# Performance work log

Hardware: AMD Instinct MI355X
Metric: run time of the kernel (lower is better)

The kernel has to match this reference:

```python
import jax, jax.numpy as jnp
import numpy as np
from jax.scipy.special import ndtr

# ---- constants matching init_kwargs ----
DF = 4.0            # fixed_df (closed-form Student-t4 quantile used)
EWMA_ALPHA = 0.94
SCALE_EPS = 1e-5
T_STEPS = 50        # diff_steps
BETA_START = 1e-4
BETA_END = 0.1
L = 6               # residual_layers
C = 32              # residual_channels
EMB = 512           # diffusion step-embedding width


def _t4_ppf(u):
    """Exact Student-t(df=4) quantile (Shaw closed form); u in (0,1)."""
    a = jnp.clip(4.0 * u * (1.0 - u), 1e-12, 1.0)
    r = jnp.sqrt(a)
    q = 2.0 * jnp.sqrt(jnp.maximum(jnp.cos(jnp.arccos(r) / 3.0) / r - 1.0, 0.0))
    return jnp.sign(u - 0.5) * q


def _forward(x_hist, z_init, noise, w_in, b_in, temb_w1, temb_b1, temb_w2, temb_b2,
             lyr_wt, lyr_bt, lyr_wdil, lyr_bdil, lyr_wout, lyr_bout,
             w_o1, b_o1, w_o2, b_o2, num_samples):
    B, Tc, D = x_hist.shape
    S = num_samples
    # ---- Student-t marginal fit (EWMA variance recurrence as lax.scan) ----
    loc = jnp.mean(x_hist, axis=1, keepdims=True)              # [B,1,D]
    c2 = (x_hist - loc) ** 2                                    # [B,Tc,D]
    def ewma_step(v, c):
        return EWMA_ALPHA * v + (1.0 - EWMA_ALPHA) * c, None
    v_last, _ = jax.lax.scan(ewma_step, c2[:, 0, :], jnp.swapaxes(c2[:, 1:, :], 0, 1))
    scale_f = jnp.maximum(jnp.sqrt(v_last * (DF - 2.0) / DF), SCALE_EPS)  # [B,D]

    # ---- DDPM schedule (linear betas) ----
    betas = jnp.linspace(BETA_START, BETA_END, T_STEPS).astype(jnp.float32)
    alphas = 1.0 - betas
    abar = jnp.cumprod(alphas)
    abar_prev = jnp.concatenate([jnp.ones((1,), jnp.float32), abar[:-1]])
    coef_x0 = betas * jnp.sqrt(abar_prev) / (1.0 - abar)
    coef_xt = (1.0 - abar_prev) * jnp.sqrt(alphas) / (1.0 - abar)
    post_var = betas * (1.0 - abar_prev) / (1.0 - abar)
    sqrt_ab = jnp.sqrt(abar)
    sqrt_1mab = jnp.sqrt(1.0 - abar)

    half = jnp.arange(64, dtype=jnp.float32)

    def eps_net(x, t):
        # diffusion-step embedding
        e = t.astype(jnp.float32) * 10.0 ** (half * 4.0 / 63.0)
        pe = jnp.concatenate([jnp.sin(e), jnp.cos(e)])          # [128]
        te = jax.nn.silu(pe @ temb_w1 + temb_b1)
        te = jax.nn.silu(te @ temb_w2 + temb_b2)                # [EMB]
        h = jax.nn.relu(jnp.einsum('cd,bdh->bch', w_in, x) + b_in[:, None])
        skip = jnp.zeros_like(h)
        for i in range(L):
            cond = te @ lyr_wt[i] + lyr_bt[i]                   # [C]
            d = 2 ** i
            y = jax.lax.conv_general_dilated(
                h + cond[None, :, None], lyr_wdil[i], (1,), [(d, d)],
                rhs_dilation=(d,), dimension_numbers=('NCH', 'OIH', 'NCH')
            ) + lyr_bdil[i][None, :, None]                       # [B,2C,H]
            gate, filt = jnp.split(y, 2, axis=1)
            y = jnp.tanh(filt) * jax.nn.sigmoid(gate)            # [B,C,H]
            y = jnp.einsum('oc,bch->boh', lyr_wout[i], y) + lyr_bout[i][None, :, None]
            res, sk = jnp.split(y, 2, axis=1)
            h = (h + res) * (1.0 / np.sqrt(2.0))
            skip = skip + sk
        s = jax.nn.relu(jnp.einsum('oc,bch->boh', w_o1, skip * (1.0 / np.sqrt(L))) + b_o1[:, None])
        return jnp.einsum('dc,bch->bdh', w_o2, s) + b_o2[:, None]

    @jax.checkpoint
    def ddpm_step(x, inp):
        t, nz = inp
        eps = eps_net(x, t)
        x0 = jnp.clip((x - sqrt_1mab[t] * eps) / sqrt_ab[t], -1.0, 1.0)  # clip_denoised
        mean = coef_x0[t] * x0 + coef_xt[t] * x
        x = mean + jnp.where(t > 0, jnp.sqrt(post_var[t]), 0.0) * nz
        return x, None

    ts = jnp.arange(T_STEPS - 1, -1, -1)
    z, _ = jax.lax.scan(ddpm_step, z_init, (ts, noise))          # [S*B,D,H]
    H = z.shape[-1]
    z = z.reshape(S, B, D, H).transpose(0, 1, 3, 2)              # [S,B,H,D]

    # ---- Gaussian -> Student-t marginal transform ----
    u = jnp.clip(ndtr(z), 1e-6, 1.0 - 1e-6)
    t_std = _t4_ppf(u)
    return loc[None] + scale_f[None, :, None, :] * t_std          # [S,B,H,D]


def setup_inputs() -> dict:
    key = jax.random.key(0)
    ks = jax.random.split(key, 12)
    D, Tc, H, B, S = 128, 192, 24, 32, 16
    p = lambda k, sh: jax.random.normal(k, sh, jnp.float32) * 0.05
    z = lambda sh: jnp.zeros(sh, jnp.float32)
    return {
        'x_hist': jax.random.normal(ks[0], (B, Tc, D), jnp.float32),
        'z_init': jax.random.normal(ks[1], (S * B, D, H), jnp.float32),
        'noise': jax.random.normal(ks[2], (T_STEPS, S * B, D, H), jnp.float32),
        'w_in': p(ks[3], (C, D)), 'b_in': z((C,)),
        'temb_w1': p(ks[4], (128, EMB)), 'temb_b1': z((EMB,)),
        'temb_w2': p(ks[5], (EMB, EMB)), 'temb_b2': z((EMB,)),
        'lyr_wt': p(ks[6], (L, EMB, C)), 'lyr_bt': z((L, C)),
        'lyr_wdil': p(ks[7], (L, 2 * C, C, 3)), 'lyr_bdil': z((L, 2 * C)),
        'lyr_wout': p(ks[8], (L, 2 * C, C)), 'lyr_bout': z((L, 2 * C)),
        'w_o1': p(ks[9], (C, C)), 'b_o1': z((C,)),
        'w_o2': p(ks[10], (D, C)), 'b_o2': z((D,)),
        'num_samples': 16,
    }


def reference(x_hist, z_init, noise, w_in, b_in, temb_w1, temb_b1, temb_w2, temb_b2,
              lyr_wt, lyr_bt, lyr_wdil, lyr_bdil, lyr_wout, lyr_bout,
              w_o1, b_o1, w_o2, b_o2, num_samples):
    return _forward(x_hist, z_init, noise, w_in, b_in, temb_w1, temb_b1, temb_w2, temb_b2,
                    lyr_wt, lyr_bt, lyr_wdil, lyr_bdil, lyr_wout, lyr_bout,
                    w_o1, b_o1, w_o2, b_o2, num_samples)
```

## Files before the change

kernel.cpp:

```cpp
#include <hip/hip_runtime.h>
#include <math.h>

#define T_STEPS 50
#define NB 512
#define RS2 0.70710678118654752f
#define INV_SQRT_L 0.40824829046386302f
#define WPACK_SHORT_OFF 36864

struct SchedArg { float cx0[T_STEPS], cxt[T_STEPS], sig[T_STEPS], s1m[T_STEPS], isab[T_STEPS]; };
struct FreqArg  { double f[64]; };

typedef short bf16x8 __attribute__((ext_vector_type(8)));
typedef float f32x4  __attribute__((ext_vector_type(4)));

__device__ __forceinline__ float4 ld4s(const float* p) { return *reinterpret_cast<const float4*>(p); }
__device__ __forceinline__ void   st4s(float* p, float4 v) { *reinterpret_cast<float4*>(p) = v; }
__device__ __forceinline__ float4 ld4g(const float* __restrict__ p) { return *reinterpret_cast<const float4*>(p); }
__device__ __forceinline__ float fast_sig(float x)  { return 1.f / (1.f + __expf(-x)); }
__device__ __forceinline__ float fast_tanh(float x) { float e = __expf(2.f * x); return 1.f - 2.f / (e + 1.f); }

__device__ __forceinline__ unsigned rne1(float f) {
    unsigned u = __float_as_uint(f);
    return (u + 0x7FFFu + ((u >> 16) & 1u)) >> 16;
}
__device__ __forceinline__ unsigned pk2(float a, float b) {
    unsigned r;
    asm("v_cvt_pk_bf16_f32 %0, %1, %2" : "=v"(r) : "v"(a), "v"(b));
    return r;
}
__device__ __forceinline__ void st_bf4(short* p, float a, float b, float c, float d) {
    uint2 v; v.x = pk2(a, b); v.y = pk2(c, d);
    *reinterpret_cast<uint2*>(p) = v;
}
__device__ __forceinline__ f32x4 mma(bf16x8 a, bf16x8 b, f32x4 c) {
    return __builtin_amdgcn_mfma_f32_16x16x32_bf16(a, b, c, 0, 0, 0);
}
__device__ __forceinline__ f32x4 bias4s(const float* p) {
    float4 b = ld4s(p);
    f32x4 r; r[0] = b.x; r[1] = b.y; r[2] = b.z; r[3] = b.w;
    return r;
}
__device__ __forceinline__ bf16x8 ldfrag(const short* p) {
    return *reinterpret_cast<const bf16x8*>(p);
}

__global__ __launch_bounds__(256) void fit_kernel(const float* __restrict__ xh,
                                                  float* __restrict__ loc,
                                                  float* __restrict__ scalef) {
    int gid = blockIdx.x * 256 + threadIdx.x;
    int b = gid >> 7, d = gid & 127;
    const float* p = xh + (size_t)b * 192 * 128 + d;
    float s = 0.f;
    for (int t = 0; t < 192; ++t) s += p[t * 128];
    float m = s * (1.0f / 192.0f);
    float v = 0.f;
    for (int t = 0; t < 192; ++t) {
        float c = p[t * 128] - m; c *= c;
        v = (t == 0) ? c : 0.94f * v + (1.0f - 0.94f) * c;
    }
    loc[gid] = m;
    scalef[gid] = fmaxf(sqrtf(v * 0.5f), 1e-5f);
}

__global__ __launch_bounds__(256) void temb_kernel(
    const float* __restrict__ w1, const float* __restrict__ b1,
    const float* __restrict__ w2, const float* __restrict__ b2,
    const float* __restrict__ wt, const float* __restrict__ bt,
    float* __restrict__ cond_all, FreqArg fq) {
    int t = blockIdx.x;
    int tid = threadIdx.x;
    __shared__ float pe[128], te1[512], te2[512];
    if (tid < 64) {
        double e = (double)t * fq.f[tid];
        pe[tid]      = (float)sin(e);
        pe[tid + 64] = (float)cos(e);
    }
    __syncthreads();
    for (int j = tid; j < 512; j += 256) {
        float acc = b1[j];
        for (int k = 0; k < 128; ++k) acc += pe[k] * w1[k * 512 + j];
        te1[j] = acc / (1.f + expf(-acc));
    }
    __syncthreads();
    for (int j = tid; j < 512; j += 256) {
        float acc = b2[j];
        for (int k = 0; k < 512; ++k) acc += te1[k] * w2[k * 512 + j];
        te2[j] = acc / (1.f + expf(-acc));
    }
    __syncthreads();
    if (tid < 192) {
        int l = tid >> 5, c = tid & 31;
        float acc = bt[l * 32 + c];
        const float* w = wt + (size_t)l * 512 * 32 + c;
        for (int k = 0; k < 512; ++k) acc += te2[k] * w[k * 32];
        cond_all[t * 192 + tid] = acc;
    }
}

__global__ __launch_bounds__(256) void prep_kernel(
    const float* __restrict__ w_in, const float* __restrict__ lyr_wdil,
    const float* __restrict__ lyr_wout, const float* __restrict__ w_o1,
    const float* __restrict__ w_o2, short* __restrict__ wpack) {
    int gid = blockIdx.x * 256 + threadIdx.x;
    if (gid >= 58368) return;
    int j = gid & 7, l = (gid >> 3) & 63, frag = gid >> 9;
    int m = l & 15, k = (l >> 4) * 8 + j;
    float v;
    if (frag < 8) {
        int m2 = frag >> 2, ks = frag & 3;
        v = w_in[(m2 * 16 + m) * 128 + ks * 32 + k];
    } else if (frag < 80) {
        int fi = frag - 8;
        int li = fi / 12, rem = fi % 12;
        int mg = rem / 6, rem2 = rem % 6;
        int tp = rem2 >> 1, gf = rem2 & 1;
        int o = gf * 32 + mg * 16 + m;
        v = lyr_wdil[((li * 64 + o) * 32 + k) * 3 + tp];
    } else if (frag < 104) {
        int fi = frag - 80;
        int li = fi >> 2, mo = fi & 3;
        v = lyr_wout[li * 2048 + (mo * 16 + m) * 32 + k];
    } else if (frag < 106) {
        int m2 = frag - 104;
        v = w_o1[(m2 * 16 + m) * 32 + k] * INV_SQRT_L;
    } else {
        int m8 = frag - 106;
        v = w_o2[(m8 * 16 + m) * 32 + k];
    }
    wpack[gid] = (short)rne1(v);
}

__global__ __launch_bounds__(256, 2) void diffusion_kernel(
    const float* __restrict__ z_init, const float* __restrict__ noise,
    const float* __restrict__ b_in,  const float* __restrict__ lyr_bdil,
    const float* __restrict__ lyr_bout, const float* __restrict__ b_o1,
    const float* __restrict__ b_o2, const float* __restrict__ cond_all,
    const short* __restrict__ wpack, const float* __restrict__ loc,
    const float* __restrict__ scalef, float* __restrict__ out, SchedArg sc) {

    __shared__ __align__(16) short xbB[32 * 136];
    __shared__ __align__(16) short hcB[33 * 40];
    __shared__ __align__(16) short actB[32 * 40];
    __shared__ __align__(16) short skB[32 * 40];
    __shared__ __align__(16) float biasB[960];
    __shared__ __align__(16) float condB[2][192];

    const int tid = threadIdx.x;
    const int wv  = __builtin_amdgcn_readfirstlane(tid >> 6);
    const int l   = tid & 63;
    const int ln  = l & 15;
    const int lq  = l >> 4;
    const int bb  = blockIdx.x;

    const short* wpP1 = wpack;
    const short* wpCv = wpack + 4096;
    const short* wpWo = wpack + 40960;
    const short* wpO1 = wpack + 53248;
    const short* wpO2 = wpack + 54272;

    const int mh   = wv >> 1;
    const int nn   = wv & 1;
    const int colw = nn * 16 + ln;
    const bool cvw = (colw < 24);

    bf16x8 aP1[4], aCv[6][3][2], aO1, aWoR[5], aWoS[6], aO2[2];
#pragma unroll
    for (int ks = 0; ks < 4; ++ks)
        aP1[ks] = ldfrag(wpP1 + (mh * 4 + ks) * 512 + l * 8);
    aO1 = ldfrag(wpO1 + mh * 512 + l * 8);
#pragma unroll
    for (int li = 0; li < 6; ++li) {
#pragma unroll
        for (int tp = 0; tp < 3; ++tp) {
            if (li == 5 && tp != 1) continue;
#pragma unroll
            for (int gf = 0; gf < 2; ++gf)
                aCv[li][tp][gf] = ldfrag(wpCv + (li * 12 + mh * 6 + tp * 2 + gf) * 512 + l * 8);
        }
        if (li < 5) aWoR[li] = ldfrag(wpWo + (li * 4 + mh) * 512 + l * 8);
        aWoS[li] = ldfrag(wpWo + (li * 4 + 2 + mh) * 512 + l * 8);
    }
    aO2[0] = ldfrag(wpO2 + wv * 512 + l * 8);
    aO2[1] = ldfrag(wpO2 + (wv + 4) * 512 + l * 8);

    for (int i = tid; i < 3072; i += 256) {
        int d = i / 24, h = i - d * 24;
        xbB[h * 136 + d] = (short)rne1(z_init[(size_t)bb * 3072 + i]);
    }
    for (int i = tid; i < 1088; i += 256) xbB[24 * 136 + i] = 0;
    for (int i = tid; i < 960; i += 256) {
        float v;
        if      (i < 32)  v = b_in[i];
        else if (i < 416) v = lyr_bdil[i - 32];
        else if (i < 800) v = lyr_bout[i - 416];
        else if (i < 832) v = b_o1[i - 800];
        else              v = b_o2[i - 832];
        biasB[i] = v;
    }
    if (tid < 192) condB[0][tid] = cond_all[(T_STEPS - 1) * 192 + tid];
    if (tid < 40) hcB[32 * 40 + tid] = 0;

    f32x4 xr[2][2];
#pragma unroll
    for (int mi = 0; mi < 2; ++mi)
#pragma unroll
        for (int n = 0; n < 2; ++n) {
            const int col = n * 16 + ln;
            const int d0 = (wv + 4 * mi) * 16 + lq * 4;
#pragma unroll
            for (int i = 0; i < 4; ++i)
                xr[mi][n][i] = (col < 24) ? z_init[(size_t)bb * 3072 + (d0 + i) * 24 + col] : 0.f;
        }
    __syncthreads();

    for (int step = 0; step < T_STEPS; ++step) {
        const int t = T_STEPS - 1 - step;
        const float* cnd = condB[step & 1];

        float cndnext = 0.f;
        if (step + 1 < T_STEPS && tid < 192)
            cndnext = cond_all[(t - 1) * 192 + tid];

        f32x4 hr;
        {
            f32x4 acc = bias4s(biasB + mh * 16 + lq * 4);
            const short* xb = xbB + colw * 136;
#pragma unroll
            for (int ks = 0; ks < 4; ++ks)
                acc = mma(aP1[ks], ldfrag(xb + ks * 32 + lq * 8), acc);
#pragma unroll
            for (int i = 0; i < 4; ++i) acc[i] = fmaxf(acc[i], 0.f);
            hr = acc;
            float4 cv = ld4s(cnd + mh * 16 + lq * 4);
            st_bf4(hcB + colw * 40 + mh * 16 + lq * 4,
                   hr[0] + cv.x, hr[1] + cv.y, hr[2] + cv.z, hr[3] + cv.w);
        }
        f32x4 skr;
#pragma unroll
        for (int i = 0; i < 4; ++i) skr[i] = 0.f;
        __syncthreads();

#pragma unroll
        for (int li = 0; li < 6; ++li) {
            const int dd = 1 << li;
            {
                f32x4 accg = bias4s(biasB + 32 + li * 64 + mh * 16 + lq * 4);
                f32x4 accf = bias4s(biasB + 32 + li * 64 + 32 + mh * 16 + lq * 4);
#pragma unroll
                for (int tp = 0; tp < 3; ++tp) {
                    if (li == 5 && tp != 1) continue;
                    int hh = colw + (tp - 1) * dd;
                    int colp = ((unsigned)hh < 24u) ? hh : 32;
                    bf16x8 b = ldfrag(hcB + colp * 40 + lq * 8);
                    accg = mma(aCv[li][tp][0], b, accg);
                    accf = mma(aCv[li][tp][1], b, accf);
                }
                st_bf4(actB + colw * 40 + mh * 16 + lq * 4,
                       fast_tanh(accf[0]) * fast_sig(accg[0]),
                       fast_tanh(accf[1]) * fast_sig(accg[1]),
                       fast_tanh(accf[2]) * fast_sig(accg[2]),
                       fast_tanh(accf[3]) * fast_sig(accg[3]));
            }
            __syncthreads();

            {
                bf16x8 b = ldfrag(actB + colw * 40 + lq * 8);
                if (li < 5) {
                    f32x4 accR = mma(aWoR[li], b,
                                     bias4s(biasB + 416 + li * 64 + mh * 16 + lq * 4));
#pragma unroll
                    for (int i = 0; i < 4; ++i) hr[i] = (hr[i] + accR[i]) * RS2;
                    float4 cv = ld4s(cnd + (li + 1) * 32 + mh * 16 + lq * 4);
                    st_bf4(hcB + colw * 40 + mh * 16 + lq * 4,
                           hr[0] + cv.x, hr[1] + cv.y, hr[2] + cv.z, hr[3] + cv.w);
                }
                f32x4 accS = mma(aWoS[li], b,
                                 bias4s(biasB + 416 + li * 64 + (2 + mh) * 16 + lq * 4));
#pragma unroll
                for (int i = 0; i < 4; ++i) skr[i] += accS[i];
                if (li == 5)
                    st_bf4(skB + colw * 40 + mh * 16 + lq * 4,
                           skr[0], skr[1], skr[2], skr[3]);
            }
            __syncthreads();
        }

        {
            f32x4 acc = bias4s(biasB + 800 + mh * 16 + lq * 4);
            acc = mma(aO1, ldfrag(skB + colw * 40 + lq * 8), acc);
            st_bf4(actB + colw * 40 + mh * 16 + lq * 4,
                   fmaxf(acc[0], 0.f), fmaxf(acc[1], 0.f),
                   fmaxf(acc[2], 0.f), fmaxf(acc[3], 0.f));
        }
        __syncthreads();

        {
            const float cx0 = sc.cx0[t], cxt = sc.cxt[t], sig = sc.sig[t];
            const float s1m = sc.s1m[t], isab = sc.isab[t];
#pragma unroll
            for (int mi = 0; mi < 2; ++mi) {
                const int d0 = (wv + 4 * mi) * 16 + lq * 4;
                f32x4 bia = bias4s(biasB + 832 + d0);
#pragma unroll
                for (int n = 0; n < 2; ++n) {
                    const int col = n * 16 + ln;
                    f32x4 acc = mma(aO2[mi], ldfrag(actB + col * 40 + lq * 8), bia);
                    if (col < 24) {
                        const float* nzp = noise + ((size_t)step * NB + bb) * 3072 + col;
                        float xn[4];
#pragma unroll
                        for (int i = 0; i < 4; ++i) {
                            float xv = xr[mi][n][i];
                            float nz = nzp[(d0 + i) * 24];
                            float x0 = fminf(fmaxf((xv - s1m * acc[i]) * isab, -1.f), 1.f);
                            xn[i] = cx0 * x0 + cxt * xv + sig * nz;
                            xr[mi][n][i] = xn[i];
                        }
                        st_bf4(xbB + col * 136 + d0, xn[0], xn[1], xn[2], xn[3]);
                    }
                }
            }
            if (step + 1 < T_STEPS && tid < 192)
                condB[(step + 1) & 1][tid] = cndnext;
        }
        __syncthreads();
    }

    {
        const int b = bb & 31;
#pragma unroll
        for (int mi = 0; mi < 2; ++mi) {
#pragma unroll
            for (int n = 0; n < 2; ++n) {
                const int col = n * 16 + ln;
                if (col >= 24) continue;
                const int d0 = (wv + 4 * mi) * 16 + lq * 4;
                float4 l4 = ld4g(loc + b * 128 + d0);
                float4 s4 = ld4g(scalef + b * 128 + d0);
                float4 o4;
#pragma unroll
                for (int e = 0; e < 4; ++e) {
                    float z = xr[mi][n][e];
                    float u = 0.5f * (1.f + erff(z * RS2));
                    u = fminf(fmaxf(u, 1e-6f), 1.f - 1e-6f);
                    float a4 = fminf(fmaxf(4.f * u * (1.f - u), 1e-12f), 1.f);
                    float rr = sqrtf(a4);
                    float q2 = 2.f * sqrtf(fmaxf(cosf(acosf(rr) * (1.f / 3.f)) / rr - 1.f, 0.f));
                    float tstd = (u < 0.5f) ? -q2 : q2;
                    (&o4.x)[e] = (&l4.x)[e] + (&s4.x)[e] * tstd;
                }
                *reinterpret_cast<float4*>(out + (size_t)bb * 3072 + col * 128 + d0) = o4;
            }
        }
    }
}

extern "C" void kernel_launch(void* const* d_in, const int* in_sizes, int n_in,
                              void* d_out, int out_size, void* d_ws, size_t ws_size,
                              hipStream_t stream) {
    const float* x_hist  = (const float*)d_in[0];
    const float* z_init  = (const float*)d_in[1];
    const float* noise   = (const float*)d_in[2];
    const float* w_in    = (const float*)d_in[3];
    const float* b_in    = (const float*)d_in[4];
    const float* temb_w1 = (const float*)d_in[5];
    const float* temb_b1 = (const float*)d_in[6];
    const float* temb_w2 = (const float*)d_in[7];
    const float* temb_b2 = (const float*)d_in[8];
    const float* lyr_wt  = (const float*)d_in[9];
    const float* lyr_bt  = (const float*)d_in[10];
    const float* lyr_wdil= (const float*)d_in[11];
    const float* lyr_bdil= (const float*)d_in[12];
    const float* lyr_wout= (const float*)d_in[13];
    const float* lyr_bout= (const float*)d_in[14];
    const float* w_o1    = (const float*)d_in[15];
    const float* b_o1    = (const float*)d_in[16];
    const float* w_o2    = (const float*)d_in[17];
    const float* b_o2    = (const float*)d_in[18];
    float* out = (float*)d_out;

    float* loc      = (float*)d_ws;
    float* scalef   = loc + 4096;
    float* cond_all = scalef + 4096;
    short* wpack    = (short*)d_ws + WPACK_SHORT_OFF;

    SchedArg sa;
    double abar = 1.0;
    for (int t = 0; t < T_STEPS; ++t) {
        double beta  = 1e-4 + (0.1 - 1e-4) * ((double)t / 49.0);
        double alpha = 1.0 - beta;
        double abprev = abar;
        abar *= alpha;
        sa.cx0[t]  = (float)(beta * sqrt(abprev) / (1.0 - abar));
        sa.cxt[t]  = (float)((1.0 - abprev) * sqrt(alpha) / (1.0 - abar));
        double pv  = beta * (1.0 - abprev) / (1.0 - abar);
        sa.sig[t]  = (t > 0) ? (float)sqrt(pv) : 0.f;
        sa.s1m[t]  = (float)sqrt(1.0 - abar);
        sa.isab[t] = (float)(1.0 / sqrt(abar));
    }
    FreqArg fa;
    for (int j = 0; j < 64; ++j) fa.f[j] = pow(10.0, (double)j * 4.0 / 63.0);

    prep_kernel<<<228, 256, 0, stream>>>(w_in, lyr_wdil, lyr_wout, w_o1, w_o2, wpack);
    fit_kernel<<<16, 256, 0, stream>>>(x_hist, loc, scalef);
    temb_kernel<<<T_STEPS, 256, 0, stream>>>(temb_w1, temb_b1, temb_w2, temb_b2,
                                             lyr_wt, lyr_bt, cond_all, fa);
    diffusion_kernel<<<NB, 256, 0, stream>>>(z_init, noise, b_in, lyr_bdil,
                                             lyr_bout, b_o1, b_o2, cond_all,
                                             wpack, loc, scalef, out, sa);
}
```

Baseline: 488.2 us.

## Process two sample rows per block to halve grid and amortize barriers

Each block now handles two independent sample/batch rows, with double LDS buffers and duplicated register state, and the grid shrinks from 512 to 256 blocks. The point is to interleave two independent MFMA chains between each pair of barriers, hiding latency and amortizing the many per-layer __syncthreads. In exchange, register pressure rises, launch bounds drop to one block per SIMD group, and only 256 blocks now cover the 256 CUs, so each CU runs a single workgroup.

```diff
diff --git a/kernel.cpp b/kernel.cpp
--- a/kernel.cpp
+++ b/kernel.cpp
@@ -14,7 +14,6 @@
 typedef float f32x4  __attribute__((ext_vector_type(4)));
 
 __device__ __forceinline__ float4 ld4s(const float* p) { return *reinterpret_cast<const float4*>(p); }
-__device__ __forceinline__ void   st4s(float* p, float4 v) { *reinterpret_cast<float4*>(p) = v; }
 __device__ __forceinline__ float4 ld4g(const float* __restrict__ p) { return *reinterpret_cast<const float4*>(p); }
 __device__ __forceinline__ float fast_sig(float x)  { return 1.f / (1.f + __expf(-x)); }
 __device__ __forceinline__ float fast_tanh(float x) { float e = __expf(2.f * x); return 1.f - 2.f / (e + 1.f); }
@@ -130,7 +129,7 @@
     wpack[gid] = (short)rne1(v);
 }
 
-__global__ __launch_bounds__(256, 2) void diffusion_kernel(
+__global__ __launch_bounds__(256, 1) void diffusion_kernel(
     const float* __restrict__ z_init, const float* __restrict__ noise,
     const float* __restrict__ b_in,  const float* __restrict__ lyr_bdil,
     const float* __restrict__ lyr_bout, const float* __restrict__ b_o1,
@@ -138,10 +137,10 @@
     const short* __restrict__ wpack, const float* __restrict__ loc,
     const float* __restrict__ scalef, float* __restrict__ out, SchedArg sc) {
 
-    __shared__ __align__(16) short xbB[32 * 136];
-    __shared__ __align__(16) short hcB[33 * 40];
-    __shared__ __align__(16) short actB[32 * 40];
-    __shared__ __align__(16) short skB[32 * 40];
+    __shared__ __align__(16) short xbB[2][32 * 136];
+    __shared__ __align__(16) short hcB[2][33 * 40];
+    __shared__ __align__(16) short actB[2][32 * 40];
+    __shared__ __align__(16) short skB[2][32 * 40];
     __shared__ __align__(16) float biasB[960];
     __shared__ __align__(16) float condB[2][192];
 
@@ -161,7 +160,6 @@
     const int mh   = wv >> 1;
     const int nn   = wv & 1;
     const int colw = nn * 16 + ln;
-    const bool cvw = (colw < 24);
 
     bf16x8 aP1[4], aCv[6][3][2], aO1, aWoR[5], aWoS[6], aO2[2];
 #pragma unroll
@@ -183,11 +181,16 @@
     aO2[0] = ldfrag(wpO2 + wv * 512 + l * 8);
     aO2[1] = ldfrag(wpO2 + (wv + 4) * 512 + l * 8);
 
-    for (int i = tid; i < 3072; i += 256) {
-        int d = i / 24, h = i - d * 24;
-        xbB[h * 136 + d] = (short)rne1(z_init[(size_t)bb * 3072 + i]);
-    }
-    for (int i = tid; i < 1088; i += 256) xbB[24 * 136 + i] = 0;
+#pragma unroll
+    for (int r = 0; r < 2; ++r) {
+        const float* zg = z_init + (size_t)(bb * 2 + r) * 3072;
+        for (int i = tid; i < 3072; i += 256) {
+            int d = i / 24, h = i - d * 24;
+            xbB[r][h * 136 + d] = (short)rne1(zg[i]);
+        }
+        for (int i = tid; i < 1088; i += 256) xbB[r][24 * 136 + i] = 0;
+        if (tid < 40) hcB[r][32 * 40 + tid] = 0;
+    }
     for (int i = tid; i < 960; i += 256) {
         float v;
         if      (i < 32)  v = b_in[i];
@@ -198,19 +201,21 @@
         biasB[i] = v;
     }
     if (tid < 192) condB[0][tid] = cond_all[(T_STEPS - 1) * 192 + tid];
-    if (tid < 40) hcB[32 * 40 + tid] = 0;
-
-    f32x4 xr[2][2];
-#pragma unroll
-    for (int mi = 0; mi < 2; ++mi)
-#pragma unroll
-        for (int n = 0; n < 2; ++n) {
-            const int col = n * 16 + ln;
-            const int d0 = (wv + 4 * mi) * 16 + lq * 4;
-#pragma unroll
-            for (int i = 0; i < 4; ++i)
-                xr[mi][n][i] = (col < 24) ? z_init[(size_t)bb * 3072 + (d0 + i) * 24 + col] : 0.f;
-        }
+
+    f32x4 xr[2][2][2];
+#pragma unroll
+    for (int r = 0; r < 2; ++r)
+#pragma unroll
+        for (int mi = 0; mi < 2; ++mi)
+#pragma unroll
+            for (int n = 0; n < 2; ++n) {
+                const int col = n * 16 + ln;
+                const int d0 = (wv + 4 * mi) * 16 + lq * 4;
+#pragma unroll
+                for (int i = 0; i < 4; ++i)
+                    xr[r][mi][n][i] = (col < 24)
+                        ? z_init[(size_t)(bb * 2 + r) * 3072 + (d0 + i) * 24 + col] : 0.f;
+            }
     __syncthreads();
 
     for (int step = 0; step < T_STEPS; ++step) {
@@ -221,76 +226,92 @@
         if (step + 1 < T_STEPS && tid < 192)
             cndnext = cond_all[(t - 1) * 192 + tid];
 
-        f32x4 hr;
+        f32x4 hr[2], skr[2];
         {
-            f32x4 acc = bias4s(biasB + mh * 16 + lq * 4);
-            const short* xb = xbB + colw * 136;
-#pragma unroll
-            for (int ks = 0; ks < 4; ++ks)
-                acc = mma(aP1[ks], ldfrag(xb + ks * 32 + lq * 8), acc);
-#pragma unroll
-            for (int i = 0; i < 4; ++i) acc[i] = fmaxf(acc[i], 0.f);
-            hr = acc;
+            f32x4 bia = bias4s(biasB + mh * 16 + lq * 4);
             float4 cv = ld4s(cnd + mh * 16 + lq * 4);
-            st_bf4(hcB + colw * 40 + mh * 16 + lq * 4,
-                   hr[0] + cv.x, hr[1] + cv.y, hr[2] + cv.z, hr[3] + cv.w);
-        }
-        f32x4 skr;
-#pragma unroll
-        for (int i = 0; i < 4; ++i) skr[i] = 0.f;
+#pragma unroll
+            for (int r = 0; r < 2; ++r) {
+                f32x4 acc = bia;
+                const short* xb = xbB[r] + colw * 136;
+#pragma unroll
+                for (int ks = 0; ks < 4; ++ks)
+                    acc = mma(aP1[ks], ldfrag(xb + ks * 32 + lq * 8), acc);
+#pragma unroll
+                for (int i = 0; i < 4; ++i) acc[i] = fmaxf(acc[i], 0.f);
+                hr[r] = acc;
+#pragma unroll
+                for (int i = 0; i < 4; ++i) skr[r][i] = 0.f;
+                st_bf4(hcB[r] + colw * 40 + mh * 16 + lq * 4,
+                       acc[0] + cv.x, acc[1] + cv.y, acc[2] + cv.z, acc[3] + cv.w);
+            }
+        }
         __syncthreads();
 
 #pragma unroll
         for (int li = 0; li < 6; ++li) {
             const int dd = 1 << li;
             {
-                f32x4 accg = bias4s(biasB + 32 + li * 64 + mh * 16 + lq * 4);
-                f32x4 accf = bias4s(biasB + 32 + li * 64 + 32 + mh * 16 + lq * 4);
-#pragma unroll
-                for (int tp = 0; tp < 3; ++tp) {
-                    if (li == 5 && tp != 1) continue;
-                    int hh = colw + (tp - 1) * dd;
-                    int colp = ((unsigned)hh < 24u) ? hh : 32;
-                    bf16x8 b = ldfrag(hcB + colp * 40 + lq * 8);
-                    accg = mma(aCv[li][tp][0], b, accg);
-                    accf = mma(aCv[li][tp][1], b, accf);
+                f32x4 bg = bias4s(biasB + 32 + li * 64 + mh * 16 + lq * 4);
+                f32x4 bf = bias4s(biasB + 32 + li * 64 + 32 + mh * 16 + lq * 4);
+#pragma unroll
+                for (int r = 0; r < 2; ++r) {
+                    f32x4 accg = bg, accf = bf;
+#pragma unroll
+                    for (int tp = 0; tp < 3; ++tp) {
+                        if (li == 5 && tp != 1) continue;
+                        int hh = colw + (tp - 1) * dd;
+                        int colp = ((unsigned)hh < 24u) ? hh : 32;
+                        bf16x8 b = ldfrag(hcB[r] + colp * 40 + lq * 8);
+                        accg = mma(aCv[li][tp][0], b, accg);
+                        accf = mma(aCv[li][tp][1], b, accf);
+                    }
+                    st_bf4(actB[r] + colw * 40 + mh * 16 + lq * 4,
+                           fast_tanh(accf[0]) * fast_sig(accg[0]),
+                           fast_tanh(accf[1]) * fast_sig(accg[1]),
+                           fast_tanh(accf[2]) * fast_sig(accg[2]),
+                           fast_tanh(accf[3]) * fast_sig(accg[3]));
                 }
-                st_bf4(actB + colw * 40 + mh * 16 + lq * 4,
-                       fast_tanh(accf[0]) * fast_sig(accg[0]),
-                       fast_tanh(accf[1]) * fast_sig(accg[1]),
-                       fast_tanh(accf[2]) * fast_sig(accg[2]),
-                       fast_tanh(accf[3]) * fast_sig(accg[3]));
             }
             __syncthreads();
 
             {
-                bf16x8 b = ldfrag(actB + colw * 40 + lq * 8);
-                if (li < 5) {
-                    f32x4 accR = mma(aWoR[li], b,
-                                     bias4s(biasB + 416 + li * 64 + mh * 16 + lq * 4));
-#pragma unroll
-                    for (int i = 0; i < 4; ++i) hr[i] = (hr[i] + accR[i]) * RS2;
-                    float4 cv = ld4s(cnd + (li + 1) * 32 + mh * 16 + lq * 4);
-                    st_bf4(hcB + colw * 40 + mh * 16 + lq * 4,
-                           hr[0] + cv.x, hr[1] + cv.y, hr[2] + cv.z, hr[3] + cv.w);
+                f32x4 bR, bS;
+                if (li < 5) bR = bias4s(biasB + 416 + li * 64 + mh * 16 + lq * 4);
+                bS = bias4s(biasB + 416 + li * 64 + (2 + mh) * 16 + lq * 4);
+                float4 cv;
+                if (li < 5) cv = ld4s(cnd + (li + 1) * 32 + mh * 16 + lq * 4);
+#pragma unroll
+                for (int r = 0; r < 2; ++r) {
+                    bf16x8 b = ldfrag(actB[r] + colw * 40 + lq * 8);
+                    if (li < 5) {
+                        f32x4 accR = mma(aWoR[li], b, bR);
+#pragma unroll
+                        for (int i = 0; i < 4; ++i) hr[r][i] = (hr[r][i] + accR[i]) * RS2;
+                        st_bf4(hcB[r] + colw * 40 + mh * 16 + lq * 4,
+                               hr[r][0] + cv.x, hr[r][1] + cv.y,
+                               hr[r][2] + cv.z, hr[r][3] + cv.w);
+                    }
+                    f32x4 accS = mma(aWoS[li], b, bS);
+#pragma unroll
+                    for (int i = 0; i < 4; ++i) skr[r][i] += accS[i];
+                    if (li == 5)
+                        st_bf4(skB[r] + colw * 40 + mh * 16 + lq * 4,
+                               skr[r][0], skr[r][1], skr[r][2], skr[r][3]);
                 }
-                f32x4 accS = mma(aWoS[li], b,
-                                 bias4s(biasB + 416 + li * 64 + (2 + mh) * 16 + lq * 4));
-#pragma unroll
-                for (int i = 0; i < 4; ++i) skr[i] += accS[i];
-                if (li == 5)
-                    st_bf4(skB + colw * 40 + mh * 16 + lq * 4,
-                           skr[0], skr[1], skr[2], skr[3]);
             }
             __syncthreads();
         }
 
         {
-            f32x4 acc = bias4s(biasB + 800 + mh * 16 + lq * 4);
-            acc = mma(aO1, ldfrag(skB + colw * 40 + lq * 8), acc);
-            st_bf4(actB + colw * 40 + mh * 16 + lq * 4,
-                   fmaxf(acc[0], 0.f), fmaxf(acc[1], 0.f),
-                   fmaxf(acc[2], 0.f), fmaxf(acc[3], 0.f));
+            f32x4 bia = bias4s(biasB + 800 + mh * 16 + lq * 4);
+#pragma unroll
+            for (int r = 0; r < 2; ++r) {
+                f32x4 acc = mma(aO1, ldfrag(skB[r] + colw * 40 + lq * 8), bia);
+                st_bf4(actB[r] + colw * 40 + mh * 16 + lq * 4,
+                       fmaxf(acc[0], 0.f), fmaxf(acc[1], 0.f),
+                       fmaxf(acc[2], 0.f), fmaxf(acc[3], 0.f));
+            }
         }
         __syncthreads();
 
@@ -298,25 +319,29 @@
             const float cx0 = sc.cx0[t], cxt = sc.cxt[t], sig = sc.sig[t];
             const float s1m = sc.s1m[t], isab = sc.isab[t];
 #pragma unroll
-            for (int mi = 0; mi < 2; ++mi) {
-                const int d0 = (wv + 4 * mi) * 16 + lq * 4;
-                f32x4 bia = bias4s(biasB + 832 + d0);
-#pragma unroll
-                for (int n = 0; n < 2; ++n) {
-                    const int col = n * 16 + ln;
-                    f32x4 acc = mma(aO2[mi], ldfrag(actB + col * 40 + lq * 8), bia);
-                    if (col < 24) {
-                        const float* nzp = noise + ((size_t)step * NB + bb) * 3072 + col;
-                        float xn[4];
-#pragma unroll
-                        for (int i = 0; i < 4; ++i) {
-                            float xv = xr[mi][n][i];
-                            float nz = nzp[(d0 + i) * 24];
-                            float x0 = fminf(fmaxf((xv - s1m * acc[i]) * isab, -1.f), 1.f);
-                            xn[i] = cx0 * x0 + cxt * xv + sig * nz;
-                            xr[mi][n][i] = xn[i];
+            for (int r = 0; r < 2; ++r) {
+                const float* nzb = noise + ((size_t)step * NB + bb * 2 + r) * 3072;
+#pragma unroll
+                for (int mi = 0; mi < 2; ++mi) {
+                    const int d0 = (wv + 4 * mi) * 16 + lq * 4;
+                    f32x4 bia = bias4s(biasB + 832 + d0);
+#pragma unroll
+                    for (int n = 0; n < 2; ++n) {
+                        const int col = n * 16 + ln;
+                        f32x4 acc = mma(aO2[mi], ldfrag(actB[r] + col * 40 + lq * 8), bia);
+                        if (col < 24) {
+                            const float* nzp = nzb + col;
+                            float xn[4];
+#pragma unroll
+                            for (int i = 0; i < 4; ++i) {
+                                float xv = xr[r][mi][n][i];
+                                float nz = nzp[(d0 + i) * 24];
+                                float x0 = fminf(fmaxf((xv - s1m * acc[i]) * isab, -1.f), 1.f);
+                                xn[i] = cx0 * x0 + cxt * xv + sig * nz;
+                                xr[r][mi][n][i] = xn[i];
+                            }
+                            st_bf4(xbB[r] + col * 136 + d0, xn[0], xn[1], xn[2], xn[3]);
                         }
-                        st_bf4(xbB + col * 136 + d0, xn[0], xn[1], xn[2], xn[3]);
                     }
                 }
             }
@@ -326,8 +351,9 @@
         __syncthreads();
     }
 
-    {
-        const int b = bb & 31;
+#pragma unroll
+    for (int r = 0; r < 2; ++r) {
+        const int b = (bb * 2 + r) & 31;
 #pragma unroll
         for (int mi = 0; mi < 2; ++mi) {
 #pragma unroll
@@ -340,7 +366,7 @@
                 float4 o4;
 #pragma unroll
                 for (int e = 0; e < 4; ++e) {
-                    float z = xr[mi][n][e];
+                    float z = xr[r][mi][n][e];
                     float u = 0.5f * (1.f + erff(z * RS2));
                     u = fminf(fmaxf(u, 1e-6f), 1.f - 1e-6f);
                     float a4 = fminf(fmaxf(4.f * u * (1.f - u), 1e-12f), 1.f);
@@ -349,7 +375,7 @@
                     float tstd = (u < 0.5f) ? -q2 : q2;
                     (&o4.x)[e] = (&l4.x)[e] + (&s4.x)[e] * tstd;
                 }
-                *reinterpret_cast<float4*>(out + (size_t)bb * 3072 + col * 128 + d0) = o4;
+                *reinterpret_cast<float4*>(out + (size_t)(bb * 2 + r) * 3072 + col * 128 + d0) = o4;
             }
         }
     }
@@ -405,7 +431,7 @@
     fit_kernel<<<16, 256, 0, stream>>>(x_hist, loc, scalef);
     temb_kernel<<<T_STEPS, 256, 0, stream>>>(temb_w1, temb_b1, temb_w2, temb_b2,
                                              lyr_wt, lyr_bt, cond_all, fa);
-    diffusion_kernel<<<NB, 256, 0, stream>>>(z_init, noise, b_in, lyr_bdil,
-                                             lyr_bout, b_o1, b_o2, cond_all,
-                                             wpack, loc, scalef, out, sa);
-}
+    diffusion_kernel<<<256, 256, 0, stream>>>(z_init, noise, b_in, lyr_bdil,
+                                              lyr_bout, b_o1, b_o2, cond_all,
+                                              wpack, loc, scalef, out, sa);
+}
```

Result: slower. 719.1 us (+47.3%).

## Restructure diffusion kernel to two waves owning full channels per column

Applied to the files above, without the earlier changes.

The diffusion kernel moves from 4 waves (each owning half the channels for 16 columns) to 2 waves that each own all channels for their 16 columns. This lets the gated activation and residual stages stay within one wave, which removes one of the two block barriers per layer and drops the barrier between layers 4 and 5. Conv weights are no longer held in registers for all layers; they are streamed per layer from global memory into double-buffered register sets, prefetched while the current layer computes. The trade-offs are fewer waves per block, 8 output MMAs per wave (with 8 of 16 lanes idle for columns past 24), and per-layer global weight reloads on every step.

```diff
diff --git a/kernel.cpp b/kernel.cpp
--- a/kernel.cpp
+++ b/kernel.cpp
@@ -14,7 +14,6 @@
 typedef float f32x4  __attribute__((ext_vector_type(4)));
 
 __device__ __forceinline__ float4 ld4s(const float* p) { return *reinterpret_cast<const float4*>(p); }
-__device__ __forceinline__ void   st4s(float* p, float4 v) { *reinterpret_cast<float4*>(p) = v; }
 __device__ __forceinline__ float4 ld4g(const float* __restrict__ p) { return *reinterpret_cast<const float4*>(p); }
 __device__ __forceinline__ float fast_sig(float x)  { return 1.f / (1.f + __expf(-x)); }
 __device__ __forceinline__ float fast_tanh(float x) { float e = __expf(2.f * x); return 1.f - 2.f / (e + 1.f); }
@@ -130,7 +129,19 @@
     wpack[gid] = (short)rne1(v);
 }
 
-__global__ __launch_bounds__(256, 2) void diffusion_kernel(
+__device__ __forceinline__ void load_conv(const short* base, int l, bf16x8* cv, bool l5) {
+#pragma unroll
+    for (int tp = 0; tp < 3; ++tp) {
+        if (l5 && tp != 1) continue;
+#pragma unroll
+        for (int mg = 0; mg < 2; ++mg)
+#pragma unroll
+            for (int gf = 0; gf < 2; ++gf)
+                cv[tp * 4 + mg * 2 + gf] = ldfrag(base + (mg * 6 + tp * 2 + gf) * 512 + l * 8);
+    }
+}
+
+__global__ __launch_bounds__(128, 1) void diffusion_kernel(
     const float* __restrict__ z_init, const float* __restrict__ noise,
     const float* __restrict__ b_in,  const float* __restrict__ lyr_bdil,
     const float* __restrict__ lyr_bout, const float* __restrict__ b_o1,
@@ -139,9 +150,8 @@
     const float* __restrict__ scalef, float* __restrict__ out, SchedArg sc) {
 
     __shared__ __align__(16) short xbB[32 * 136];
-    __shared__ __align__(16) short hcB[33 * 40];
-    __shared__ __align__(16) short actB[32 * 40];
-    __shared__ __align__(16) short skB[32 * 40];
+    __shared__ __align__(16) short hcB[2][33 * 40];
+    __shared__ __align__(16) short trB[32 * 40];
     __shared__ __align__(16) float biasB[960];
     __shared__ __align__(16) float condB[2][192];
 
@@ -151,6 +161,8 @@
     const int ln  = l & 15;
     const int lq  = l >> 4;
     const int bb  = blockIdx.x;
+    const int colw = wv * 16 + ln;
+    const bool cvw = (colw < 24);
 
     const short* wpP1 = wpack;
     const short* wpCv = wpack + 4096;
@@ -158,37 +170,31 @@
     const short* wpO1 = wpack + 53248;
     const short* wpO2 = wpack + 54272;
 
-    const int mh   = wv >> 1;
-    const int nn   = wv & 1;
-    const int colw = nn * 16 + ln;
-    const bool cvw = (colw < 24);
-
-    bf16x8 aP1[4], aCv[6][3][2], aO1, aWoR[5], aWoS[6], aO2[2];
-#pragma unroll
-    for (int ks = 0; ks < 4; ++ks)
-        aP1[ks] = ldfrag(wpP1 + (mh * 4 + ks) * 512 + l * 8);
-    aO1 = ldfrag(wpO1 + mh * 512 + l * 8);
-#pragma unroll
-    for (int li = 0; li < 6; ++li) {
-#pragma unroll
-        for (int tp = 0; tp < 3; ++tp) {
-            if (li == 5 && tp != 1) continue;
-#pragma unroll
-            for (int gf = 0; gf < 2; ++gf)
-                aCv[li][tp][gf] = ldfrag(wpCv + (li * 12 + mh * 6 + tp * 2 + gf) * 512 + l * 8);
-        }
-        if (li < 5) aWoR[li] = ldfrag(wpWo + (li * 4 + mh) * 512 + l * 8);
-        aWoS[li] = ldfrag(wpWo + (li * 4 + 2 + mh) * 512 + l * 8);
-    }
-    aO2[0] = ldfrag(wpO2 + wv * 512 + l * 8);
-    aO2[1] = ldfrag(wpO2 + (wv + 4) * 512 + l * 8);
-
-    for (int i = tid; i < 3072; i += 256) {
+    bf16x8 aP1[2][4], aWo[6][4], aO1[2], aO2[8];
+#pragma unroll
+    for (int m = 0; m < 2; ++m) {
+#pragma unroll
+        for (int ks = 0; ks < 4; ++ks)
+            aP1[m][ks] = ldfrag(wpP1 + (m * 4 + ks) * 512 + l * 8);
+        aO1[m] = ldfrag(wpO1 + m * 512 + l * 8);
+    }
+#pragma unroll
+    for (int li = 0; li < 6; ++li)
+#pragma unroll
+        for (int mo = 0; mo < 4; ++mo)
+            aWo[li][mo] = ldfrag(wpWo + (li * 4 + mo) * 512 + l * 8);
+#pragma unroll
+    for (int m8 = 0; m8 < 8; ++m8) aO2[m8] = ldfrag(wpO2 + m8 * 512 + l * 8);
+
+    bf16x8 cvA[12], cvB[12];
+    load_conv(wpCv, l, cvA, false);
+
+    for (int i = tid; i < 3072; i += 128) {
         int d = i / 24, h = i - d * 24;
         xbB[h * 136 + d] = (short)rne1(z_init[(size_t)bb * 3072 + i]);
     }
-    for (int i = tid; i < 1088; i += 256) xbB[24 * 136 + i] = 0;
-    for (int i = tid; i < 960; i += 256) {
+    for (int i = tid; i < 1088; i += 128) xbB[24 * 136 + i] = 0;
+    for (int i = tid; i < 960; i += 128) {
         float v;
         if      (i < 32)  v = b_in[i];
         else if (i < 416) v = lyr_bdil[i - 32];
@@ -197,160 +203,177 @@
         else              v = b_o2[i - 832];
         biasB[i] = v;
     }
-    if (tid < 192) condB[0][tid] = cond_all[(T_STEPS - 1) * 192 + tid];
-    if (tid < 40) hcB[32 * 40 + tid] = 0;
-
-    f32x4 xr[2][2];
-#pragma unroll
-    for (int mi = 0; mi < 2; ++mi)
-#pragma unroll
-        for (int n = 0; n < 2; ++n) {
-            const int col = n * 16 + ln;
-            const int d0 = (wv + 4 * mi) * 16 + lq * 4;
-#pragma unroll
-            for (int i = 0; i < 4; ++i)
-                xr[mi][n][i] = (col < 24) ? z_init[(size_t)bb * 3072 + (d0 + i) * 24 + col] : 0.f;
-        }
+    for (int i = tid; i < 192; i += 128) condB[0][i] = cond_all[(T_STEPS - 1) * 192 + i];
+    if (tid < 40) { hcB[0][32 * 40 + tid] = 0; hcB[1][32 * 40 + tid] = 0; }
+
+    f32x4 xr[8];
+#pragma unroll
+    for (int m8 = 0; m8 < 8; ++m8) {
+        const int d0 = m8 * 16 + lq * 4;
+#pragma unroll
+        for (int i = 0; i < 4; ++i)
+            xr[m8][i] = cvw ? z_init[(size_t)bb * 3072 + (d0 + i) * 24 + colw] : 0.f;
+    }
     __syncthreads();
+
+    f32x4 hr[2], skr[2];
+
+#define LAYER(LI, CV, CVN, NLI)                                                          \
+    {                                                                                    \
+        const int dd = 1 << LI;                                                          \
+        f32x4 ac00 = bias4s(biasB + 32 + LI * 64 + lq * 4);                \
+        f32x4 ac01 = bias4s(biasB + 32 + LI * 64 + 32 + lq * 4);           \
+        f32x4 ac10 = bias4s(biasB + 32 + LI * 64 + 16 + lq * 4);           \
+        f32x4 ac11 = bias4s(biasB + 32 + LI * 64 + 48 + lq * 4);           \
+        const short* hb = hcB[LI & 1];                                                   \
+        _Pragma("unroll")                                                                \
+        for (int tp = 0; tp < 3; ++tp) {                                                 \
+            if (LI == 5 && tp != 1) continue;                                            \
+            int hh = colw + (tp - 1) * dd;                                               \
+            int colp = ((unsigned)hh < 24u) ? hh : 32;                                   \
+            bf16x8 b = ldfrag(hb + colp * 40 + lq * 8);                                  \
+            ac00 = mma(CV[tp * 4 + 0], b, ac00);                                         \
+            ac01 = mma(CV[tp * 4 + 1], b, ac01);                                         \
+            ac10 = mma(CV[tp * 4 + 2], b, ac10);                                         \
+            ac11 = mma(CV[tp * 4 + 3], b, ac11);                                         \
+        }                                                                                \
+        load_conv(wpCv + (NLI) * 12 * 512, l, CVN, (NLI) == 5);                          \
+        st_bf4(trB + colw * 40 + lq * 4,                                                 \
+               fast_tanh(ac01[0]) * fast_sig(ac00[0]),                                   \
+               fast_tanh(ac01[1]) * fast_sig(ac00[1]),                                   \
+               fast_tanh(ac01[2]) * fast_sig(ac00[2]),                                   \
+               fast_tanh(ac01[3]) * fast_sig(ac00[3]));                                  \
+        st_bf4(trB + colw * 40 + 16 + lq * 4,                                            \
+               fast_tanh(ac11[0]) * fast_sig(ac10[0]),                                   \
+               fast_tanh(ac11[1]) * fast_sig(ac10[1]),                                   \
+               fast_tanh(ac11[2]) * fast_sig(ac10[2]),                                   \
+               fast_tanh(ac11[3]) * fast_sig(ac10[3]));                                  \
+        bf16x8 b2 = ldfrag(trB + colw * 40 + lq * 8);                                    \
+        if (LI < 5) {                                                                    \
+            f32x4 aR0 = mma(aWo[LI][0], b2, bias4s(biasB + 416 + LI * 64 + lq * 4));     \
+            f32x4 aR1 = mma(aWo[LI][1], b2, bias4s(biasB + 416 + LI * 64 + 16 + lq * 4));\
+            _Pragma("unroll")                                                            \
+            for (int i = 0; i < 4; ++i) {                                                \
+                hr[0][i] = (hr[0][i] + aR0[i]) * RS2;                                    \
+                hr[1][i] = (hr[1][i] + aR1[i]) * RS2;                                    \
+            }                                                                            \
+            float4 c0 = ld4s(cnd + (LI + 1) * 32 + lq * 4);                              \
+            float4 c1 = ld4s(cnd + (LI + 1) * 32 + 16 + lq * 4);                         \
+            short* hn = hcB[(LI + 1) & 1];                                               \
+            st_bf4(hn + colw * 40 + lq * 4,                                              \
+                   hr[0][0] + c0.x, hr[0][1] + c0.y, hr[0][2] + c0.z, hr[0][3] + c0.w);  \
+            st_bf4(hn + colw * 40 + 16 + lq * 4,                                         \
+                   hr[1][0] + c1.x, hr[1][1] + c1.y, hr[1][2] + c1.z, hr[1][3] + c1.w);  \
+        }                                                                                \
+        f32x4 aS0 = mma(aWo[LI][2], b2, bias4s(biasB + 416 + LI * 64 + 32 + lq * 4));    \
+        f32x4 aS1 = mma(aWo[LI][3], b2, bias4s(biasB + 416 + LI * 64 + 48 + lq * 4));    \
+        _Pragma("unroll")                                                                \
+        for (int i = 0; i < 4; ++i) { skr[0][i] += aS0[i]; skr[1][i] += aS1[i]; }        \
+    }
 
     for (int step = 0; step < T_STEPS; ++step) {
         const int t = T_STEPS - 1 - step;
         const float* cnd = condB[step & 1];
 
-        float cndnext = 0.f;
-        if (step + 1 < T_STEPS && tid < 192)
-            cndnext = cond_all[(t - 1) * 192 + tid];
-
-        f32x4 hr;
+        float cn0 = 0.f, cn1 = 0.f;
+        if (step + 1 < T_STEPS) {
+            cn0 = cond_all[(t - 1) * 192 + tid];
+            if (tid < 64) cn1 = cond_all[(t - 1) * 192 + 128 + tid];
+        }
+
+#pragma unroll
+        for (int m = 0; m < 2; ++m) {
+            f32x4 acc = bias4s(biasB + m * 16 + lq * 4);
+            const short* xb = xbB + colw * 136;
+#pragma unroll
+            for (int ks = 0; ks < 4; ++ks)
+                acc = mma(aP1[m][ks], ldfrag(xb + ks * 32 + lq * 8), acc);
+#pragma unroll
+            for (int i = 0; i < 4; ++i) { acc[i] = fmaxf(acc[i], 0.f); skr[m][i] = 0.f; }
+            hr[m] = acc;
+            float4 cv = ld4s(cnd + m * 16 + lq * 4);
+            st_bf4(hcB[0] + colw * 40 + m * 16 + lq * 4,
+                   acc[0] + cv.x, acc[1] + cv.y, acc[2] + cv.z, acc[3] + cv.w);
+        }
+        __syncthreads();
+
+        LAYER(0, cvA, cvB, 1)
+        __syncthreads();
+        LAYER(1, cvB, cvA, 2)
+        __syncthreads();
+        LAYER(2, cvA, cvB, 3)
+        __syncthreads();
+        LAYER(3, cvB, cvA, 4)
+        __syncthreads();
+        LAYER(4, cvA, cvB, 5)
+        LAYER(5, cvB, cvA, 0)
+
         {
-            f32x4 acc = bias4s(biasB + mh * 16 + lq * 4);
-            const short* xb = xbB + colw * 136;
-#pragma unroll
-            for (int ks = 0; ks < 4; ++ks)
-                acc = mma(aP1[ks], ldfrag(xb + ks * 32 + lq * 8), acc);
-#pragma unroll
-            for (int i = 0; i < 4; ++i) acc[i] = fmaxf(acc[i], 0.f);
-            hr = acc;
-            float4 cv = ld4s(cnd + mh * 16 + lq * 4);
-            st_bf4(hcB + colw * 40 + mh * 16 + lq * 4,
-                   hr[0] + cv.x, hr[1] + cv.y, hr[2] + cv.z, hr[3] + cv.w);
+#pragma unroll
+            for (int m = 0; m < 2; ++m)
+                st_bf4(trB + colw * 40 + m * 16 + lq * 4,
+                       skr[m][0], skr[m][1], skr[m][2], skr[m][3]);
+            bf16x8 b = ldfrag(trB + colw * 40 + lq * 8);
+#pragma unroll
+            for (int m = 0; m < 2; ++m) {
+                f32x4 acc = mma(aO1[m], b, bias4s(biasB + 800 + m * 16 + lq * 4));
+                st_bf4(trB + colw * 40 + m * 16 + lq * 4,
+                       fmaxf(acc[0], 0.f), fmaxf(acc[1], 0.f),
+                       fmaxf(acc[2], 0.f), fmaxf(acc[3], 0.f));
+            }
         }
-        f32x4 skr;
-#pragma unroll
-        for (int i = 0; i < 4; ++i) skr[i] = 0.f;
-        __syncthreads();
-
-#pragma unroll
-        for (int li = 0; li < 6; ++li) {
-            const int dd = 1 << li;
-            {
-                f32x4 accg = bias4s(biasB + 32 + li * 64 + mh * 16 + lq * 4);
-                f32x4 accf = bias4s(biasB + 32 + li * 64 + 32 + mh * 16 + lq * 4);
-#pragma unroll
-                for (int tp = 0; tp < 3; ++tp) {
-                    if (li == 5 && tp != 1) continue;
-                    int hh = colw + (tp - 1) * dd;
-                    int colp = ((unsigned)hh < 24u) ? hh : 32;
-                    bf16x8 b = ldfrag(hcB + colp * 40 + lq * 8);
-                    accg = mma(aCv[li][tp][0], b, accg);
-                    accf = mma(aCv[li][tp][1], b, accf);
-                }
-                st_bf4(actB + colw * 40 + mh * 16 + lq * 4,
-                       fast_tanh(accf[0]) * fast_sig(accg[0]),
-                       fast_tanh(accf[1]) * fast_sig(accg[1]),
-                       fast_tanh(accf[2]) * fast_sig(accg[2]),
-                       fast_tanh(accf[3]) * fast_sig(accg[3]));
-            }
-            __syncthreads();
-
-            {
-                bf16x8 b = ldfrag(actB + colw * 40 + lq * 8);
-                if (li < 5) {
-                    f32x4 accR = mma(aWoR[li], b,
-                                     bias4s(biasB + 416 + li * 64 + mh * 16 + lq * 4));
-#pragma unroll
-                    for (int i = 0; i < 4; ++i) hr[i] = (hr[i] + accR[i]) * RS2;
-                    float4 cv = ld4s(cnd + (li + 1) * 32 + mh * 16 + lq * 4);
-                    st_bf4(hcB + colw * 40 + mh * 16 + lq * 4,
-                           hr[0] + cv.x, hr[1] + cv.y, hr[2] + cv.z, hr[3] + cv.w);
-                }
-                f32x4 accS = mma(aWoS[li], b,
-                                 bias4s(biasB + 416 + li * 64 + (2 + mh) * 16 + lq * 4));
-#pragma unroll
-                for (int i = 0; i < 4; ++i) skr[i] += accS[i];
-                if (li == 5)
-                    st_bf4(skB + colw * 40 + mh * 16 + lq * 4,
-                           skr[0], skr[1], skr[2], skr[3]);
-            }
-            __syncthreads();
-        }
 
         {
-            f32x4 acc = bias4s(biasB + 800 + mh * 16 + lq * 4);
-            acc = mma(aO1, ldfrag(skB + colw * 40 + lq * 8), acc);
-            st_bf4(actB + colw * 40 + mh * 16 + lq * 4,
-                   fmaxf(acc[0], 0.f), fmaxf(acc[1], 0.f),
-                   fmaxf(acc[2], 0.f), fmaxf(acc[3], 0.f));
-        }
-        __syncthreads();
-
-        {
+            bf16x8 b = ldfrag(trB + colw * 40 + lq * 8);
             const float cx0 = sc.cx0[t], cxt = sc.cxt[t], sig = sc.sig[t];
             const float s1m = sc.s1m[t], isab = sc.isab[t];
-#pragma unroll
-            for (int mi = 0; mi < 2; ++mi) {
-                const int d0 = (wv + 4 * mi) * 16 + lq * 4;
-                f32x4 bia = bias4s(biasB + 832 + d0);
-#pragma unroll
-                for (int n = 0; n < 2; ++n) {
-                    const int col = n * 16 + ln;
-                    f32x4 acc = mma(aO2[mi], ldfrag(actB + col * 40 + lq * 8), bia);
-                    if (col < 24) {
-                        const float* nzp = noise + ((size_t)step * NB + bb) * 3072 + col;
-                        float xn[4];
-#pragma unroll
-                        for (int i = 0; i < 4; ++i) {
-                            float xv = xr[mi][n][i];
-                            float nz = nzp[(d0 + i) * 24];
-                            float x0 = fminf(fmaxf((xv - s1m * acc[i]) * isab, -1.f), 1.f);
-                            xn[i] = cx0 * x0 + cxt * xv + sig * nz;
-                            xr[mi][n][i] = xn[i];
-                        }
-                        st_bf4(xbB + col * 136 + d0, xn[0], xn[1], xn[2], xn[3]);
+            const float* nzp = noise + ((size_t)step * NB + bb) * 3072 + (cvw ? colw : 0);
+#pragma unroll
+            for (int m8 = 0; m8 < 8; ++m8) {
+                const int d0 = m8 * 16 + lq * 4;
+                f32x4 acc = mma(aO2[m8], b, bias4s(biasB + 832 + d0));
+                if (cvw) {
+                    float xn[4];
+#pragma unroll
+                    for (int i = 0; i < 4; ++i) {
+                        float xv = xr[m8][i];
+                        float nz = nzp[(d0 + i) * 24];
+                        float x0 = fminf(fmaxf((xv - s1m * acc[i]) * isab, -1.f), 1.f);
+                        xn[i] = cx0 * x0 + cxt * xv + sig * nz;
+                        xr[m8][i] = xn[i];
                     }
+                    st_bf4(xbB + colw * 136 + d0, xn[0], xn[1], xn[2], xn[3]);
                 }
             }
-            if (step + 1 < T_STEPS && tid < 192)
-                condB[(step + 1) & 1][tid] = cndnext;
+            if (step + 1 < T_STEPS) {
+                condB[(step + 1) & 1][tid] = cn0;
+                if (tid < 64) condB[(step + 1) & 1][128 + tid] = cn1;
+            }
         }
         __syncthreads();
     }
-
-    {
+#undef LAYER
+
+    if (cvw) {
         const int b = bb & 31;
 #pragma unroll
-        for (int mi = 0; mi < 2; ++mi) {
-#pragma unroll
-            for (int n = 0; n < 2; ++n) {
-                const int col = n * 16 + ln;
-                if (col >= 24) continue;
-                const int d0 = (wv + 4 * mi) * 16 + lq * 4;
-                float4 l4 = ld4g(loc + b * 128 + d0);
-                float4 s4 = ld4g(scalef + b * 128 + d0);
-                float4 o4;
-#pragma unroll
-                for (int e = 0; e < 4; ++e) {
-                    float z = xr[mi][n][e];
-                    float u = 0.5f * (1.f + erff(z * RS2));
-                    u = fminf(fmaxf(u, 1e-6f), 1.f - 1e-6f);
-                    float a4 = fminf(fmaxf(4.f * u * (1.f - u), 1e-12f), 1.f);
-                    float rr = sqrtf(a4);
-                    float q2 = 2.f * sqrtf(fmaxf(cosf(acosf(rr) * (1.f / 3.f)) / rr - 1.f, 0.f));
-                    float tstd = (u < 0.5f) ? -q2 : q2;
-                    (&o4.x)[e] = (&l4.x)[e] + (&s4.x)[e] * tstd;
-                }
-                *reinterpret_cast<float4*>(out + (size_t)bb * 3072 + col * 128 + d0) = o4;
+        for (int m8 = 0; m8 < 8; ++m8) {
+            const int d0 = m8 * 16 + lq * 4;
+            float4 l4 = ld4g(loc + b * 128 + d0);
+            float4 s4 = ld4g(scalef + b * 128 + d0);
+            float4 o4;
+#pragma unroll
+            for (int e = 0; e < 4; ++e) {
+                float z = xr[m8][e];
+                float u = 0.5f * (1.f + erff(z * RS2));
+                u = fminf(fmaxf(u, 1e-6f), 1.f - 1e-6f);
+                float a4 = fminf(fmaxf(4.f * u * (1.f - u), 1e-12f), 1.f);
+                float rr = sqrtf(a4);
+                float q2 = 2.f * sqrtf(fmaxf(cosf(acosf(rr) * (1.f / 3.f)) / rr - 1.f, 0.f));
+                float tstd = (u < 0.5f) ? -q2 : q2;
+                (&o4.x)[e] = (&l4.x)[e] + (&s4.x)[e] * tstd;
             }
+            *reinterpret_cast<float4*>(out + (size_t)bb * 3072 + colw * 128 + d0) = o4;
         }
     }
 }
@@ -405,7 +428,7 @@
     fit_kernel<<<16, 256, 0, stream>>>(x_hist, loc, scalef);
     temb_kernel<<<T_STEPS, 256, 0, stream>>>(temb_w1, temb_b1, temb_w2, temb_b2,
                                              lyr_wt, lyr_bt, cond_all, fa);
-    diffusion_kernel<<<NB, 256, 0, stream>>>(z_init, noise, b_in, lyr_bdil,
+    diffusion_kernel<<<NB, 128, 0, stream>>>(z_init, noise, b_in, lyr_bdil,
                                              lyr_bout, b_o1, b_o2, cond_all,
                                              wpack, loc, scalef, out, sa);
 }
```

Result: slower. 673.9 us (+38.0%).
